# Optimization experiments

Measured on AMD Instinct MI355X. Metric: run time of the kernel, lower is better.

## Reference

```python
import jax, jax.numpy as jnp
import numpy as np
from jax import lax

B = 256; N_LAB = 20000; M = 3; D = 768
T = 5; K = 8; H = 256; DI = 512; S = 16; R = 16; NL = 4; KC = 4


def setup_inputs() -> dict:
    key = jax.random.key(0)
    ks = jax.random.split(key, 16)
    sc = 0.02
    return {
        "unlabeled_embeddings": jax.random.normal(ks[0], (B, M, D), jnp.float32),
        "labeled_embeddings": jax.random.normal(ks[1], (N_LAB, M, D), jnp.float32),
        "labeled_traits": jax.random.uniform(ks[2], (N_LAB, T), jnp.float32),
        "modality_logits": jax.random.normal(ks[3], (T, M), jnp.float32),
        "Wp": jax.random.normal(ks[4], (D + 1, H), jnp.float32) * sc,
        "bp": jnp.zeros((H,), jnp.float32),
        "ln_g": jnp.ones((NL, H), jnp.float32),
        "ln_b": jnp.zeros((NL, H), jnp.float32),
        "Win": jax.random.normal(ks[5], (NL, H, 2 * DI), jnp.float32) * sc,
        "conv_w": jax.random.normal(ks[6], (NL, DI, KC), jnp.float32) * sc,
        "conv_b": jnp.zeros((NL, DI), jnp.float32),
        "Wx": jax.random.normal(ks[7], (NL, DI, R + 2 * S), jnp.float32) * sc,
        "Wdt": jax.random.normal(ks[8], (NL, R, DI), jnp.float32) * sc,
        "bdt": jnp.full((NL, DI), -4.6, jnp.float32),
        "A_log": jnp.log(jnp.broadcast_to(jnp.arange(1, S + 1, dtype=jnp.float32), (NL, DI, S))),
        "Dp": jnp.ones((NL, DI), jnp.float32),
        "Wout": jax.random.normal(ks[9], (NL, DI, H), jnp.float32) * sc,
        "W1": jax.random.normal(ks[10], (H, H // 2), jnp.float32) * sc,
        "b1": jnp.zeros((H // 2,), jnp.float32),
        "W2": jax.random.normal(ks[11], (H // 2, 1), jnp.float32) * sc,
        "b2": jnp.zeros((1,), jnp.float32),
    }


def layer_norm(x, g, b, eps=1e-5):
    m = x.mean(-1, keepdims=True)
    v = ((x - m) ** 2).mean(-1, keepdims=True)
    return (x - m) * lax.rsqrt(v + eps) * g + b


def select_neighbors(lab_e, lab_t, unl_e, mlog):
    # Per-trait modality-weighted cosine similarity k-NN.
    w = jax.nn.softmax(mlog, axis=-1)                       # (T,M)
    q = jnp.einsum('tm,bmd->btd', w, unl_e)                 # (B,T,D)
    kk = jnp.einsum('tm,nmd->ntd', w, lab_e)                # (N,T,D)
    qn = q * lax.rsqrt(jnp.sum(q * q, -1, keepdims=True) + 1e-8)
    kn = kk * lax.rsqrt(jnp.sum(kk * kk, -1, keepdims=True) + 1e-8)
    sim = jnp.einsum('btd,ntd->btn', qn, kn)                # (B,T,N)
    _, idx = lax.top_k(sim, K)                              # (B,T,K) int32
    ne = lab_e[idx]                                         # (B,T,K,M,D)
    tg = lab_t[idx]                                         # (B,T,K,T)
    nt = jnp.diagonal(tg, axis1=1, axis2=3).transpose(0, 2, 1)  # (B,T,K)
    return ne, nt, idx


def mamba_block(x, Win, conv_w, conv_b, Wx, Wdt, bdt, A_log, Dp, Wout):
    # x: (N, L, H). Selective SSM (Mamba) block with internal residual.
    N, L, _ = x.shape
    xz = x @ Win                                            # (N,L,2*DI)
    xc, z = jnp.split(xz, 2, axis=-1)
    xp = jnp.pad(xc, ((0, 0), (KC - 1, 0), (0, 0)))         # causal depthwise conv, k=4
    xc = sum(xp[:, j:j + L, :] * conv_w[:, j] for j in range(KC)) + conv_b
    xc = jax.nn.silu(xc)
    dbl = xc @ Wx                                           # (N,L,R+2S)
    dt, Bm, Cm = jnp.split(dbl, [R, R + S], axis=-1)
    dt = jax.nn.softplus(dt @ Wdt + bdt)                    # (N,L,DI)
    A = -jnp.exp(A_log)                                     # (DI,S)
    dA = jnp.exp(dt[..., None] * A)                         # (N,L,DI,S)
    dBx = dt[..., None] * Bm[:, :, None, :] * xc[..., None] # (N,L,DI,S)

    def step(h, inp):
        a, bx = inp
        h = a * h + bx
        return h, h

    h0 = jnp.zeros((N, DI, S), x.dtype)
    _, hs = lax.scan(step, h0, (jnp.swapaxes(dA, 0, 1), jnp.swapaxes(dBx, 0, 1)))
    hs = jnp.swapaxes(hs, 0, 1)                             # (N,L,DI,S)
    y = jnp.einsum('nlds,nls->nld', hs, Cm) + Dp * xc
    y = y * jax.nn.silu(z)
    return x + y @ Wout


def _forward(unl, lab_e, lab_t, mlog, Wp, bp, ln_g, ln_b, Win, conv_w, conv_b, Wx,
             Wdt, bdt, A_log, Dp, Wout, W1, b1, W2, b2):
    ne, nt, _ = select_neighbors(lab_e, lab_t, unl, mlog)
    ne = ne.mean(3)                                         # (B,T,K,D) mean over modalities
    uc = unl.mean(1)                                        # (B,D)
    feats = jnp.concatenate([ne, jnp.broadcast_to(uc[:, None, None, :], (B, T, 1, D))], axis=2)
    tt = jnp.concatenate([nt[..., None], jnp.zeros((B, T, 1, 1), lab_t.dtype)], axis=2)
    toks = jnp.concatenate([feats, tt], axis=-1).reshape(B * T, K + 1, D + 1)
    x = toks @ Wp + bp                                      # (B*T, K+1, H)
    for i in range(NL):
        xn = layer_norm(x, ln_g[i], ln_b[i])
        x = mamba_block(xn, Win[i], conv_w[i], conv_b[i], Wx[i], Wdt[i], bdt[i],
                        A_log[i], Dp[i], Wout[i])
    ms = x[:, -1, :]                                        # masked-trait token state
    h1 = jax.nn.relu(ms @ W1 + b1)
    return (h1 @ W2 + b2).reshape(B, T)


def reference(unlabeled_embeddings, labeled_embeddings, labeled_traits, modality_logits,
              Wp, bp, ln_g, ln_b, Win, conv_w, conv_b, Wx, Wdt, bdt, A_log, Dp, Wout,
              W1, b1, W2, b2):
    return _forward(unlabeled_embeddings, labeled_embeddings, labeled_traits,
                    modality_logits, Wp, bp, ln_g, ln_b, Win, conv_w, conv_b, Wx,
                    Wdt, bdt, A_log, Dp, Wout, W1, b1, W2, b2)
```

## Files before the change

kernel.cpp:

```cpp
#include <hip/hip_runtime.h>
#include <math.h>

#define B_   256
#define NLAB 20000
#define M_   3
#define D_   768
#define T_   5
#define K_   8
#define H_   256
#define DI_  512
#define S_   16
#define R_   16
#define NL_  4
#define KC_  4
#define L_   9
#define NBT  1280
#define NROW 11520

typedef __attribute__((ext_vector_type(8))) short bf16x8;
typedef __attribute__((ext_vector_type(4))) float floatx4;


__device__ __forceinline__ float block_reduce_sum(float v) {
    __shared__ float red[4];
    int lane = threadIdx.x & 63;
    int wid  = threadIdx.x >> 6;
#pragma unroll
    for (int o = 32; o > 0; o >>= 1) v += __shfl_down(v, o);
    if (lane == 0) red[wid] = v;
    __syncthreads();
    int nw = (int)(blockDim.x >> 6);
    float r = 0.f;
#pragma unroll
    for (int i = 0; i < 4; ++i) if (i < nw) r += red[i];
    __syncthreads();
    return r;
}

__device__ __forceinline__ float sigmoidf_(float x) { return 1.f / (1.f + expf(-x)); }
__device__ __forceinline__ float siluf_(float x)    { return x * sigmoidf_(x); }
__device__ __forceinline__ float softplusf_(float x){ return x > 20.f ? x : log1pf(expf(x)); }

__device__ __forceinline__ unsigned short f2bf(float x) {
    unsigned u = __float_as_uint(x);
    unsigned r = (u + 0x7fffu + ((u >> 16) & 1u)) >> 16;
    return (unsigned short)r;
}
__device__ __forceinline__ float bf2f(unsigned short h) {
    return __uint_as_float(((unsigned)h) << 16);
}


__global__ void k_softmax_w(const float* __restrict__ mlog, float* __restrict__ w) {
    int t = threadIdx.x;
    if (t < T_) {
        float a = mlog[t*M_+0], b = mlog[t*M_+1], c = mlog[t*M_+2];
        float mx = fmaxf(a, fmaxf(b, c));
        float ea = expf(a-mx), eb = expf(b-mx), ec = expf(c-mx);
        float s = ea + eb + ec;
        w[t*M_+0] = ea/s; w[t*M_+1] = eb/s; w[t*M_+2] = ec/s;
    }
}

__global__ __launch_bounds__(256) void k_qn_uc(const float* __restrict__ unl,
                                               const float* __restrict__ w,
                                               unsigned short* __restrict__ qnh,
                                               unsigned short* __restrict__ qnl,
                                               float* __restrict__ uc) {
    int b = blockIdx.x, tid = threadIdx.x;
    float e[3][3];
#pragma unroll
    for (int c = 0; c < 3; ++c) {
        int d = tid + c*256;
#pragma unroll
        for (int m = 0; m < 3; ++m)
            e[c][m] = unl[((size_t)b*3 + m)*D_ + d];
    }
#pragma unroll
    for (int c = 0; c < 3; ++c)
        uc[(size_t)b*D_ + tid + c*256] = (e[c][0] + e[c][1] + e[c][2]) * (1.f/3.f);
    for (int t = 0; t < T_; ++t) {
        float w0 = w[t*3+0], w1 = w[t*3+1], w2 = w[t*3+2];
        float q[3]; float ss = 0.f;
#pragma unroll
        for (int c = 0; c < 3; ++c) {
            q[c] = w0*e[c][0] + w1*e[c][1] + w2*e[c][2];
            ss += q[c]*q[c];
        }
        float tot = block_reduce_sum(ss);
        float inv = rsqrtf(tot + 1e-8f);
#pragma unroll
        for (int c = 0; c < 3; ++c) {
            float v = q[c]*inv;
            size_t o = ((size_t)t*B_ + b)*D_ + tid + c*256;
            unsigned short h = f2bf(v);
            qnh[o] = h; qnl[o] = f2bf(v - bf2f(h));
        }
    }
}

__global__ __launch_bounds__(512) void k_simf(const unsigned short* __restrict__ qnh,
                                              const unsigned short* __restrict__ qnl,
                                              const float* __restrict__ lab_e,
                                              const float* __restrict__ w,
                                              float* __restrict__ sim) {
    __shared__ unsigned short Bh[128*40], Bl[128*40];
    __shared__ float rnl[128];
    int bn = blockIdx.x * 128;
    int t  = blockIdx.y;
    float w0 = w[t*3+0], w1 = w[t*3+1], w2 = w[t*3+2];
    int tid = threadIdx.x;
    int lane = tid & 63, wv = tid >> 6;
    int mbase = (wv >> 1)*64, nbase = (wv & 1)*64;
    int fr = lane & 15, kg = lane >> 4;

    int gr0 = tid >> 3, gr1 = 64 + (tid >> 3), kq = tid & 7;
    int gn0 = bn + gr0, gn1 = bn + gr1;
    bool v0 = gn0 < NLAB, v1 = gn1 < NLAB;
    const float* bp0 = lab_e + (size_t)gn0*(3*D_) + kq*4;
    const float* bp1 = lab_e + (size_t)gn1*(3*D_) + kq*4;

    floatx4 acc[4][4];
#pragma unroll
    for (int mi = 0; mi < 4; ++mi)
#pragma unroll
        for (int ni = 0; ni < 4; ++ni)
            acc[mi][ni] = (floatx4){0.f, 0.f, 0.f, 0.f};

    float ss0 = 0.f, ss1 = 0.f;
    float4 rb0[3], rb1[3];
    float4 z4 = make_float4(0.f, 0.f, 0.f, 0.f);
    rb0[0]=rb0[1]=rb0[2]=z4; rb1[0]=rb1[1]=rb1[2]=z4;
    if (v0) { rb0[0] = *(const float4*)(bp0);
              rb0[1] = *(const float4*)(bp0 + D_);
              rb0[2] = *(const float4*)(bp0 + 2*D_); }
    if (v1) { rb1[0] = *(const float4*)(bp1);
              rb1[1] = *(const float4*)(bp1 + D_);
              rb1[2] = *(const float4*)(bp1 + 2*D_); }

    for (int kt = 0; kt < 24; ++kt) {
        int k0 = kt*32;
        float4 s0, s1;
        s0.x = w0*rb0[0].x + w1*rb0[1].x + w2*rb0[2].x;
        s0.y = w0*rb0[0].y + w1*rb0[1].y + w2*rb0[2].y;
        s0.z = w0*rb0[0].z + w1*rb0[1].z + w2*rb0[2].z;
        s0.w = w0*rb0[0].w + w1*rb0[1].w + w2*rb0[2].w;
        s1.x = w0*rb1[0].x + w1*rb1[1].x + w2*rb1[2].x;
        s1.y = w0*rb1[0].y + w1*rb1[1].y + w2*rb1[2].y;
        s1.z = w0*rb1[0].z + w1*rb1[1].z + w2*rb1[2].z;
        s1.w = w0*rb1[0].w + w1*rb1[1].w + w2*rb1[2].w;
        ss0 += s0.x*s0.x + s0.y*s0.y + s0.z*s0.z + s0.w*s0.w;
        ss1 += s1.x*s1.x + s1.y*s1.y + s1.z*s1.z + s1.w*s1.w;
        ushort4 h0, l0, h1, l1;
        h0.x = f2bf(s0.x); l0.x = f2bf(s0.x - bf2f(h0.x));
        h0.y = f2bf(s0.y); l0.y = f2bf(s0.y - bf2f(h0.y));
        h0.z = f2bf(s0.z); l0.z = f2bf(s0.z - bf2f(h0.z));
        h0.w = f2bf(s0.w); l0.w = f2bf(s0.w - bf2f(h0.w));
        h1.x = f2bf(s1.x); l1.x = f2bf(s1.x - bf2f(h1.x));
        h1.y = f2bf(s1.y); l1.y = f2bf(s1.y - bf2f(h1.y));
        h1.z = f2bf(s1.z); l1.z = f2bf(s1.z - bf2f(h1.z));
        h1.w = f2bf(s1.w); l1.w = f2bf(s1.w - bf2f(h1.w));

        __syncthreads();
        *(ushort4*)(Bh + gr0*40 + kq*4) = h0;
        *(ushort4*)(Bl + gr0*40 + kq*4) = l0;
        *(ushort4*)(Bh + gr1*40 + kq*4) = h1;
        *(ushort4*)(Bl + gr1*40 + kq*4) = l1;
        if (kt < 23) {
            const float* p0 = bp0 + k0 + 32;
            const float* p1 = bp1 + k0 + 32;
            if (v0) { rb0[0] = *(const float4*)(p0);
                      rb0[1] = *(const float4*)(p0 + D_);
                      rb0[2] = *(const float4*)(p0 + 2*D_); }
            if (v1) { rb1[0] = *(const float4*)(p1);
                      rb1[1] = *(const float4*)(p1 + D_);
                      rb1[2] = *(const float4*)(p1 + 2*D_); }
        }
        __syncthreads();

        bf16x8 bhf[4], blf[4];
#pragma unroll
        for (int ni = 0; ni < 4; ++ni) {
            int off = (nbase + ni*16 + fr)*40 + kg*8;
            bhf[ni] = *(const bf16x8*)(Bh + off);
            blf[ni] = *(const bf16x8*)(Bl + off);
        }
#pragma unroll
        for (int mi = 0; mi < 4; ++mi) {
            size_t ga = ((size_t)t*B_ + (mbase + mi*16 + fr))*D_ + k0 + kg*8;
            bf16x8 ahf = *(const bf16x8*)(qnh + ga);
            bf16x8 alf = *(const bf16x8*)(qnl + ga);
#pragma unroll
            for (int ni = 0; ni < 4; ++ni) {
                floatx4 c = acc[mi][ni];
                c = __builtin_amdgcn_mfma_f32_16x16x32_bf16(ahf, bhf[ni], c, 0, 0, 0);
                c = __builtin_amdgcn_mfma_f32_16x16x32_bf16(alf, bhf[ni], c, 0, 0, 0);
                c = __builtin_amdgcn_mfma_f32_16x16x32_bf16(ahf, blf[ni], c, 0, 0, 0);
                acc[mi][ni] = c;
            }
        }
    }

    float t0 = ss0, t1 = ss1;
#pragma unroll
    for (int m = 1; m <= 4; m <<= 1) { t0 += __shfl_xor(t0, m); t1 += __shfl_xor(t1, m); }
    if ((tid & 7) == 0) {
        rnl[tid >> 3]        = rsqrtf(t0 + 1e-8f);
        rnl[64 + (tid >> 3)] = rsqrtf(t1 + 1e-8f);
    }
    __syncthreads();

    float* st = sim + (size_t)t*B_*NLAB;
#pragma unroll
    for (int mi = 0; mi < 4; ++mi) {
        int m = mbase + mi*16 + kg*4;
#pragma unroll
        for (int ni = 0; ni < 4; ++ni) {
            int nl = nbase + ni*16 + fr;
            int n = bn + nl;
            if (n < NLAB) {
                float rv = rnl[nl];
#pragma unroll
                for (int r = 0; r < 4; ++r)
                    st[(size_t)(m + r)*NLAB + n] = acc[mi][ni][r] * rv;
            }
        }
    }
}

__global__ __launch_bounds__(256) void k_topk(const float* __restrict__ sim,
                                              int* __restrict__ idx_out) {
    int b = blockIdx.x;
    int t = blockIdx.y;
    int tid = threadIdx.x;
    const float* row = sim + ((size_t)t*B_ + b)*NLAB;
    float tv[8]; int ti[8];
#pragma unroll
    for (int k = 0; k < 8; ++k) { tv[k] = -3e38f; ti[k] = 0x7fffffff; }
    for (int n = tid; n < NLAB; n += 256) {
        float v = row[n];
        if (v > tv[7]) {
            tv[7] = v; ti[7] = n;
#pragma unroll
            for (int k = 7; k > 0; --k) {
                if (tv[k] > tv[k-1]) {
                    float fv = tv[k]; tv[k] = tv[k-1]; tv[k-1] = fv;
                    int fi = ti[k]; ti[k] = ti[k-1]; ti[k-1] = fi;
                }
            }
        }
    }
    __shared__ float sv[2048];
    __shared__ int   si[2048];
    __shared__ float pv[256];
    __shared__ int   pi[256];
    __shared__ int   pp[256];
#pragma unroll
    for (int k = 0; k < 8; ++k) { sv[tid*8+k] = tv[k]; si[tid*8+k] = ti[k]; }
    __syncthreads();
    for (int r = 0; r < 8; ++r) {
        float bv = -3e38f; int bi = 0x7fffffff; int bp = 0;
#pragma unroll
        for (int k = 0; k < 8; ++k) {
            int p = tid*8 + k;
            float v = sv[p]; int ii = si[p];
            if (v > bv || (v == bv && ii < bi)) { bv = v; bi = ii; bp = p; }
        }
        pv[tid] = bv; pi[tid] = bi; pp[tid] = bp;
        __syncthreads();
        for (int off = 128; off > 0; off >>= 1) {
            if (tid < off) {
                if (pv[tid+off] > pv[tid] || (pv[tid+off] == pv[tid] && pi[tid+off] < pi[tid])) {
                    pv[tid] = pv[tid+off]; pi[tid] = pi[tid+off]; pp[tid] = pp[tid+off];
                }
            }
            __syncthreads();
        }
        if (tid == 0) {
            idx_out[((size_t)b*T_ + t)*K_ + r] = pi[0];
            sv[pp[0]] = -3e38f;
        }
        __syncthreads();
    }
}

__global__ __launch_bounds__(256) void k_toks(const float* __restrict__ lab_e,
                                              const float* __restrict__ lab_t,
                                              const float* __restrict__ uc,
                                              const int* __restrict__ idx,
                                              unsigned short* __restrict__ tokh,
                                              unsigned short* __restrict__ tokl,
                                              float* __restrict__ tt) {
    int g = blockIdx.x;
    int bt = g / L_, l = g % L_;
    int b = bt / T_, t = bt % T_;
    size_t ro = (size_t)g*D_;
    if (l < K_) {
        int n = idx[(size_t)bt*K_ + l];
        for (int d = threadIdx.x; d < D_; d += 256) {
            size_t base = (size_t)n*(3*D_) + d;
            float v = (lab_e[base] + lab_e[base + D_] + lab_e[base + 2*D_]) * (1.f/3.f);
            unsigned short h = f2bf(v);
            tokh[ro + d] = h; tokl[ro + d] = f2bf(v - bf2f(h));
        }
        if (threadIdx.x == 0) tt[g] = lab_t[(size_t)n*T_ + t];
    } else {
        for (int d = threadIdx.x; d < D_; d += 256) {
            float v = uc[(size_t)b*D_ + d];
            unsigned short h = f2bf(v);
            tokh[ro + d] = h; tokl[ro + d] = f2bf(v - bf2f(h));
        }
        if (threadIdx.x == 0) tt[g] = 0.f;
    }
}

__global__ void k_cvtw(const float* __restrict__ W,
                       unsigned short* __restrict__ th,
                       unsigned short* __restrict__ tl,
                       int Kd, int N) {
    int total = Kd * N;
    for (int id = blockIdx.x*256 + threadIdx.x; id < total; id += gridDim.x*256) {
        int n = id / Kd, k = id - n*Kd;
        float v = W[(size_t)k*N + n];
        unsigned short h = f2bf(v);
        th[id] = h; tl[id] = f2bf(v - bf2f(h));
    }
}

template<bool ADD, bool BIAS, bool TRAIT>
__global__ __launch_bounds__(256) void k_mgemm(const unsigned short* __restrict__ ah,
                                               const unsigned short* __restrict__ al,
                                               const unsigned short* __restrict__ bh,
                                               const unsigned short* __restrict__ bl,
                                               const float* __restrict__ bias,
                                               const float* __restrict__ wtrait,
                                               const float* __restrict__ tt,
                                               float* __restrict__ C,
                                               int N, int Kd) {
    __shared__ unsigned short Ah[128*40], Al[128*40], Bh[64*40], Bl[64*40];
    int bn = blockIdx.x * 64;
    int bm = blockIdx.y * 128;
    int tid = threadIdx.x;
    int lane = tid & 63, wv = tid >> 6;
    int mbase = (wv >> 1)*64, nbase = (wv & 1)*32;
    int fr = lane & 15, kg = lane >> 4;
    floatx4 acc[4][2];
#pragma unroll
    for (int mi = 0; mi < 4; ++mi)
#pragma unroll
        for (int ni = 0; ni < 2; ++ni)
            acc[mi][ni] = (floatx4){0.f, 0.f, 0.f, 0.f};

    for (int k0 = 0; k0 < Kd; k0 += 32) {
#pragma unroll
        for (int f = 0; f < 2; ++f) {
            int v = f*256 + tid;
            int r = v >> 2, kq = v & 3;
            size_t g = (size_t)(bm + r)*Kd + k0 + kq*8;
            int off = r*40 + kq*8;
            *(int4*)(Ah + off) = *(const int4*)(ah + g);
            *(int4*)(Al + off) = *(const int4*)(al + g);
        }
        {
            int r = tid >> 2, kq = tid & 3;
            size_t g = (size_t)(bn + r)*Kd + k0 + kq*8;
            int off = r*40 + kq*8;
            *(int4*)(Bh + off) = *(const int4*)(bh + g);
            *(int4*)(Bl + off) = *(const int4*)(bl + g);
        }
        __syncthreads();

        bf16x8 bhf[2], blf[2];
#pragma unroll
        for (int ni = 0; ni < 2; ++ni) {
            int off = (nbase + ni*16 + fr)*40 + kg*8;
            bhf[ni] = *(const bf16x8*)(Bh + off);
            blf[ni] = *(const bf16x8*)(Bl + off);
        }
#pragma unroll
        for (int mi = 0; mi < 4; ++mi) {
            int off = (mbase + mi*16 + fr)*40 + kg*8;
            bf16x8 ahf = *(const bf16x8*)(Ah + off);
            bf16x8 alf = *(const bf16x8*)(Al + off);
#pragma unroll
            for (int ni = 0; ni < 2; ++ni) {
                floatx4 c = acc[mi][ni];
                c = __builtin_amdgcn_mfma_f32_16x16x32_bf16(ahf, bhf[ni], c, 0, 0, 0);
                c = __builtin_amdgcn_mfma_f32_16x16x32_bf16(alf, bhf[ni], c, 0, 0, 0);
                c = __builtin_amdgcn_mfma_f32_16x16x32_bf16(ahf, blf[ni], c, 0, 0, 0);
                acc[mi][ni] = c;
            }
        }
        __syncthreads();
    }
#pragma unroll
    for (int mi = 0; mi < 4; ++mi) {
        int m0 = bm + mbase + mi*16 + kg*4;
#pragma unroll
        for (int ni = 0; ni < 2; ++ni) {
            int n = bn + nbase + ni*16 + fr;
#pragma unroll
            for (int r = 0; r < 4; ++r) {
                float v = acc[mi][ni][r];
                if (TRAIT) v += tt[m0 + r] * wtrait[n];
                if (BIAS)  v += bias[n];
                size_t o = (size_t)(m0 + r)*N + n;
                if (ADD) C[o] += v; else C[o] = v;
            }
        }
    }
}

__global__ __launch_bounds__(256) void k_ln(const float* __restrict__ x,
                                            const float* __restrict__ g,
                                            const float* __restrict__ b,
                                            float* __restrict__ xn,
                                            unsigned short* __restrict__ xnh,
                                            unsigned short* __restrict__ xnl) {
    int row = blockIdx.x, tid = threadIdx.x;
    float v = x[(size_t)row*H_ + tid];
    float mean = block_reduce_sum(v) * (1.f/H_);
    float d = v - mean;
    float var = block_reduce_sum(d*d) * (1.f/H_);
    float o = d * rsqrtf(var + 1e-5f) * g[tid] + b[tid];
    size_t oo = (size_t)row*H_ + tid;
    xn[oo] = o;
    unsigned short h = f2bf(o);
    xnh[oo] = h; xnl[oo] = f2bf(o - bf2f(h));
}

__global__ __launch_bounds__(512) void k_mamba(const float* __restrict__ xz,
                                               const float* __restrict__ cw,
                                               const float* __restrict__ cb,
                                               const unsigned short* __restrict__ wxh,
                                               const unsigned short* __restrict__ wxl,
                                               const float* __restrict__ Wdt,
                                               const float* __restrict__ bdt,
                                               const float* __restrict__ A_log,
                                               const float* __restrict__ Dp,
                                               unsigned short* __restrict__ yh,
                                               unsigned short* __restrict__ yl) {
    __shared__ float xcS[L_][516];
    __shared__ float dblS[L_][48];
    int n = blockIdx.x, d = threadIdx.x;

    float c0 = cw[d*4+0], c1 = cw[d*4+1], c2 = cw[d*4+2], c3 = cw[d*4+3];
    float bb = cb[d];
    const float* src = xz + (size_t)n*L_*(2*DI_) + d;
    float xc[L_], z[L_];
    float x0 = 0.f, x1 = 0.f, x2 = 0.f;
#pragma unroll
    for (int l = 0; l < L_; ++l) {
        float x3 = src[l*(2*DI_)];
        z[l]     = src[l*(2*DI_) + DI_];
        float s = bb + c0*x0 + c1*x1 + c2*x2 + c3*x3;
        float v = siluf_(s);
        xc[l] = v; xcS[l][d] = v;
        x0 = x1; x1 = x2; x2 = x3;
    }
    __syncthreads();

    int wv = d >> 6, lane = d & 63;
    if (wv < 3) {
        int fr = lane & 15, kg = lane >> 4;
        const unsigned short* bph = wxh + (size_t)(wv*16 + fr)*DI_;
        const unsigned short* bpl = wxl + (size_t)(wv*16 + fr)*DI_;
        floatx4 c = (floatx4){0.f, 0.f, 0.f, 0.f};
        for (int k0 = 0; k0 < DI_; k0 += 32) {
            int kb = k0 + kg*8;
            float av[8];
            if (fr < L_) {
                float4 q0 = *(const float4*)(&xcS[fr][kb]);
                float4 q1 = *(const float4*)(&xcS[fr][kb+4]);
                av[0]=q0.x; av[1]=q0.y; av[2]=q0.z; av[3]=q0.w;
                av[4]=q1.x; av[5]=q1.y; av[6]=q1.z; av[7]=q1.w;
            } else {
#pragma unroll
                for (int j = 0; j < 8; ++j) av[j] = 0.f;
            }
            bf16x8 ah, al;
#pragma unroll
            for (int j = 0; j < 8; ++j) {
                unsigned short hh = f2bf(av[j]);
                ah[j] = (short)hh;
                al[j] = (short)f2bf(av[j] - bf2f(hh));
            }
            bf16x8 bhf = *(const bf16x8*)(bph + kb);
            bf16x8 blf = *(const bf16x8*)(bpl + kb);
            c = __builtin_amdgcn_mfma_f32_16x16x32_bf16(ah, bhf, c, 0, 0, 0);
            c = __builtin_amdgcn_mfma_f32_16x16x32_bf16(al, bhf, c, 0, 0, 0);
            c = __builtin_amdgcn_mfma_f32_16x16x32_bf16(ah, blf, c, 0, 0, 0);
        }
#pragma unroll
        for (int r = 0; r < 4; ++r) {
            int row = kg*4 + r;
            if (row < L_) dblS[row][wv*16 + fr] = c[r];
        }
    }
    __syncthreads();

    float a[S_], wdt[R_];
#pragma unroll
    for (int s = 0; s < S_; ++s) a[s] = -expf(A_log[(size_t)d*S_ + s]);
#pragma unroll
    for (int r = 0; r < R_; ++r) wdt[r] = Wdt[(size_t)r*DI_ + d];
    float bdtv = bdt[d], dp = Dp[d];
    float h[S_];
#pragma unroll
    for (int s = 0; s < S_; ++s) h[s] = 0.f;
    size_t ob = (size_t)n*L_*DI_ + d;
#pragma unroll
    for (int l = 0; l < L_; ++l) {
        float s = bdtv;
#pragma unroll
        for (int r = 0; r < R_; ++r) s = fmaf(dblS[l][r], wdt[r], s);
        float dtv = softplusf_(s);
        float xcv = xc[l];
        float accv = 0.f;
#pragma unroll
        for (int si = 0; si < S_; ++si) {
            float Bv = dblS[l][16 + si], Cv = dblS[l][32 + si];
            h[si] = expf(dtv*a[si])*h[si] + dtv*Bv*xcv;
            accv = fmaf(h[si], Cv, accv);
        }
        float yv = (accv + dp*xcv) * siluf_(z[l]);
        unsigned short hh = f2bf(yv);
        yh[ob + (size_t)l*DI_] = hh;
        yl[ob + (size_t)l*DI_] = f2bf(yv - bf2f(hh));
    }
}

__global__ __launch_bounds__(128) void k_head(const float* __restrict__ x,
                                              const float* __restrict__ W1,
                                              const float* __restrict__ b1,
                                              const float* __restrict__ W2,
                                              const float* __restrict__ b2,
                                              float* __restrict__ out) {
    int n = blockIdx.x, tid = threadIdx.x;
    __shared__ float ms[H_];
    const float* src = x + ((size_t)n*L_ + (L_-1))*H_;
    ms[tid] = src[tid];
    ms[tid+128] = src[tid+128];
    __syncthreads();
    float s = b1[tid];
#pragma unroll 8
    for (int k = 0; k < H_; ++k) s = fmaf(ms[k], W1[(size_t)k*128 + tid], s);
    float h = fmaxf(s, 0.f);
    float p = h * W2[tid];
    float tot = block_reduce_sum(p);
    if (tid == 0) out[n] = tot + b2[0];
}


extern "C" void kernel_launch(void* const* d_in, const int* in_sizes, int n_in,
                              void* d_out, int out_size, void* d_ws, size_t ws_size,
                              hipStream_t stream) {
    const float* unl   = (const float*)d_in[0];
    const float* lab_e = (const float*)d_in[1];
    const float* lab_t = (const float*)d_in[2];
    const float* mlog  = (const float*)d_in[3];
    const float* Wp    = (const float*)d_in[4];
    const float* bp    = (const float*)d_in[5];
    const float* ln_g  = (const float*)d_in[6];
    const float* ln_b  = (const float*)d_in[7];
    const float* Win   = (const float*)d_in[8];
    const float* conv_w= (const float*)d_in[9];
    const float* conv_b= (const float*)d_in[10];
    const float* Wx    = (const float*)d_in[11];
    const float* Wdt   = (const float*)d_in[12];
    const float* bdt   = (const float*)d_in[13];
    const float* A_log = (const float*)d_in[14];
    const float* Dp    = (const float*)d_in[15];
    const float* Wout  = (const float*)d_in[16];
    const float* W1    = (const float*)d_in[17];
    const float* b1    = (const float*)d_in[18];
    const float* W2    = (const float*)d_in[19];
    const float* b2    = (const float*)d_in[20];

    float* ws = (float*)d_ws;
    float* w    = ws + 0;
    int*   idx  = (int*)(ws + 16);
    float* uc   = ws + 10256;
    unsigned short* wxth = (unsigned short*)(ws + 206864);
    unsigned short* wxtl = (unsigned short*)(ws + 256016);
    float* tt   = ws + 306864;
    unsigned short* qnh   = (unsigned short*)(ws + 318384);
    unsigned short* qnl   = (unsigned short*)(ws + 809904);
    unsigned short* wph   = (unsigned short*)(ws + 1301424);
    unsigned short* wpl   = (unsigned short*)(ws + 1399728);
    unsigned short* winh  = (unsigned short*)(ws + 1498032);
    unsigned short* winl  = (unsigned short*)(ws + 2022320);
    unsigned short* wouth = (unsigned short*)(ws + 2546608);
    unsigned short* woutl = (unsigned short*)(ws + 2808752);
    float* xa   = ws + 3070896;
    float* xb   = ws + 6020016;
    unsigned short* xnh   = (unsigned short*)(ws + 8969136);
    unsigned short* xnl   = (unsigned short*)(ws + 10443696);
    float* simreg = ws + 18369456;
    float* sim  = simreg;
    float* xz   = simreg;
    unsigned short* tokh = (unsigned short*)(simreg + 11796480);
    unsigned short* tokl = (unsigned short*)(simreg + 16220160);
    unsigned short* yh   = (unsigned short*)(simreg + 17694720);
    unsigned short* yl   = (unsigned short*)(simreg + 20643840);

    k_softmax_w<<<1, 64, 0, stream>>>(mlog, w);
    k_qn_uc<<<B_, 256, 0, stream>>>(unl, w, qnh, qnl, uc);
    k_cvtw<<<(768*256 + 255)/256, 256, 0, stream>>>(Wp, wph, wpl, 768, 256);
    for (int i = 0; i < NL_; ++i) {
        k_cvtw<<<(256*1024 + 255)/256, 256, 0, stream>>>(Win + (size_t)i*H_*(2*DI_),
                                                         winh + (size_t)i*H_*(2*DI_),
                                                         winl + (size_t)i*H_*(2*DI_), 256, 1024);
        k_cvtw<<<(512*256 + 255)/256, 256, 0, stream>>>(Wout + (size_t)i*DI_*H_,
                                                        wouth + (size_t)i*DI_*H_,
                                                        woutl + (size_t)i*DI_*H_, 512, 256);
        k_cvtw<<<(512*48 + 255)/256, 256, 0, stream>>>(Wx + (size_t)i*DI_*48,
                                                       wxth + (size_t)i*48*DI_,
                                                       wxtl + (size_t)i*48*DI_, 512, 48);
    }
    {
        dim3 g((NLAB + 127) / 128, T_);
        k_simf<<<g, 512, 0, stream>>>(qnh, qnl, lab_e, w, sim);
    }
    {
        dim3 g(B_, T_);
        k_topk<<<g, 256, 0, stream>>>(sim, idx);
    }
    k_toks<<<NROW, 256, 0, stream>>>(lab_e, lab_t, uc, idx, tokh, tokl, tt);
    {
        dim3 g(H_/64, NROW/128);
        k_mgemm<false,true,true><<<g, 256, 0, stream>>>(tokh, tokl, wph, wpl,
                                                        bp, Wp + (size_t)768*H_, tt, xa, H_, D_);
    }
    float* cur = xa;
    float* oth = xb;
    for (int i = 0; i < NL_; ++i) {
        k_ln<<<NROW, 256, 0, stream>>>(cur, ln_g + (size_t)i*H_, ln_b + (size_t)i*H_, oth, xnh, xnl);
        {
            dim3 g((2*DI_)/64, NROW/128);
            k_mgemm<false,false,false><<<g, 256, 0, stream>>>(xnh, xnl,
                winh + (size_t)i*H_*(2*DI_), winl + (size_t)i*H_*(2*DI_),
                nullptr, nullptr, nullptr, xz, 2*DI_, H_);
        }
        k_mamba<<<NBT, 512, 0, stream>>>(xz,
                                         conv_w + (size_t)i*DI_*KC_, conv_b + (size_t)i*DI_,
                                         wxth + (size_t)i*48*DI_, wxtl + (size_t)i*48*DI_,
                                         Wdt + (size_t)i*R_*DI_, bdt + (size_t)i*DI_,
                                         A_log + (size_t)i*DI_*S_, Dp + (size_t)i*DI_,
                                         yh, yl);
        {
            dim3 g(H_/64, NROW/128);
            k_mgemm<true,false,false><<<g, 256, 0, stream>>>(yh, yl,
                wouth + (size_t)i*DI_*H_, woutl + (size_t)i*DI_*H_,
                nullptr, nullptr, nullptr, oth, H_, DI_);
        }
        float* tmp = cur; cur = oth; oth = tmp;
    }
    k_head<<<NBT, 128, 0, stream>>>(cur, W1, b1, W2, b2, (float*)d_out);
}
```

Measured before the change: 1.521 ms.

## Double-buffer LDS in similarity GEMM, prefetch A fragments, remap blocks per XCD

```diff
diff --git a/kernel.cpp b/kernel.cpp
--- a/kernel.cpp
+++ b/kernel.cpp
@@ -50,6 +50,11 @@
     return __uint_as_float(((unsigned)h) << 16);
 }
 
+__device__ __forceinline__ void barrier_lds_only() {
+    asm volatile("s_waitcnt lgkmcnt(0)" ::: "memory");
+    __builtin_amdgcn_s_barrier();
+}
+
 
 __global__ void k_softmax_w(const float* __restrict__ mlog, float* __restrict__ w) {
     int t = threadIdx.x;
@@ -99,15 +104,40 @@
     }
 }
 
-__global__ __launch_bounds__(512) void k_simf(const unsigned short* __restrict__ qnh,
-                                              const unsigned short* __restrict__ qnl,
-                                              const float* __restrict__ lab_e,
-                                              const float* __restrict__ w,
-                                              float* __restrict__ sim) {
-    __shared__ unsigned short Bh[128*40], Bl[128*40];
+__device__ __forceinline__ void cvt_store4(const float4* rb, float w0, float w1, float w2,
+                                           unsigned short* bh, unsigned short* bl,
+                                           int off, float& ss) {
+    float4 s;
+    s.x = w0*rb[0].x + w1*rb[1].x + w2*rb[2].x;
+    s.y = w0*rb[0].y + w1*rb[1].y + w2*rb[2].y;
+    s.z = w0*rb[0].z + w1*rb[1].z + w2*rb[2].z;
+    s.w = w0*rb[0].w + w1*rb[1].w + w2*rb[2].w;
+    ss += s.x*s.x + s.y*s.y + s.z*s.z + s.w*s.w;
+    ushort4 h, l;
+    h.x = f2bf(s.x); l.x = f2bf(s.x - bf2f(h.x));
+    h.y = f2bf(s.y); l.y = f2bf(s.y - bf2f(h.y));
+    h.z = f2bf(s.z); l.z = f2bf(s.z - bf2f(h.z));
+    h.w = f2bf(s.w); l.w = f2bf(s.w - bf2f(h.w));
+    *(ushort4*)(bh + off) = h;
+    *(ushort4*)(bl + off) = l;
+}
+
+__global__ __launch_bounds__(512, 4) void k_simf(const unsigned short* __restrict__ qnh,
+                                                 const unsigned short* __restrict__ qnl,
+                                                 const float* __restrict__ lab_e,
+                                                 const float* __restrict__ w,
+                                                 float* __restrict__ sim) {
+    __shared__ unsigned short Bh[2*128*40], Bl[2*128*40];
     __shared__ float rnl[128];
-    int bn = blockIdx.x * 128;
-    int t  = blockIdx.y;
+    int bid = blockIdx.x;
+    int xcd = bid & 7, s = bid >> 3;
+    int cnt = (xcd < 5) ? 20 : 19;
+    if (s >= cnt * 5) return;
+    int start = (xcd < 5) ? xcd*20 : 100 + (xcd-5)*19;
+    int bnc = start + s / 5;
+    int t = s - (s/5)*5;
+    int bn = bnc * 128;
+
     float w0 = w[t*3+0], w1 = w[t*3+1], w2 = w[t*3+2];
     int tid = threadIdx.x;
     int lane = tid & 63, wv = tid >> 6;
@@ -137,35 +167,26 @@
     if (v1) { rb1[0] = *(const float4*)(bp1);
               rb1[1] = *(const float4*)(bp1 + D_);
               rb1[2] = *(const float4*)(bp1 + 2*D_); }
+    cvt_store4(rb0, w0, w1, w2, Bh, Bl, gr0*40 + kq*4, ss0);
+    cvt_store4(rb1, w0, w1, w2, Bh, Bl, gr1*40 + kq*4, ss1);
+
+    const unsigned short* aph = qnh + ((size_t)t*B_ + mbase + fr)*D_ + kg*8;
+    const unsigned short* apl = qnl + ((size_t)t*B_ + mbase + fr)*D_ + kg*8;
 
     for (int kt = 0; kt < 24; ++kt) {
+        int cur = kt & 1;
+        const unsigned short* bhr = Bh + cur*5120;
+        const unsigned short* blr = Bl + cur*5120;
+        unsigned short* bhw = Bh + (cur^1)*5120;
+        unsigned short* blw = Bl + (cur^1)*5120;
         int k0 = kt*32;
-        float4 s0, s1;
-        s0.x = w0*rb0[0].x + w1*rb0[1].x + w2*rb0[2].x;
-        s0.y = w0*rb0[0].y + w1*rb0[1].y + w2*rb0[2].y;
-        s0.z = w0*rb0[0].z + w1*rb0[1].z + w2*rb0[2].z;
-        s0.w = w0*rb0[0].w + w1*rb0[1].w + w2*rb0[2].w;
-        s1.x = w0*rb1[0].x + w1*rb1[1].x + w2*rb1[2].x;
-        s1.y = w0*rb1[0].y + w1*rb1[1].y + w2*rb1[2].y;
-        s1.z = w0*rb1[0].z + w1*rb1[1].z + w2*rb1[2].z;
-        s1.w = w0*rb1[0].w + w1*rb1[1].w + w2*rb1[2].w;
-        ss0 += s0.x*s0.x + s0.y*s0.y + s0.z*s0.z + s0.w*s0.w;
-        ss1 += s1.x*s1.x + s1.y*s1.y + s1.z*s1.z + s1.w*s1.w;
-        ushort4 h0, l0, h1, l1;
-        h0.x = f2bf(s0.x); l0.x = f2bf(s0.x - bf2f(h0.x));
-        h0.y = f2bf(s0.y); l0.y = f2bf(s0.y - bf2f(h0.y));
-        h0.z = f2bf(s0.z); l0.z = f2bf(s0.z - bf2f(h0.z));
-        h0.w = f2bf(s0.w); l0.w = f2bf(s0.w - bf2f(h0.w));
-        h1.x = f2bf(s1.x); l1.x = f2bf(s1.x - bf2f(h1.x));
-        h1.y = f2bf(s1.y); l1.y = f2bf(s1.y - bf2f(h1.y));
-        h1.z = f2bf(s1.z); l1.z = f2bf(s1.z - bf2f(h1.z));
-        h1.w = f2bf(s1.w); l1.w = f2bf(s1.w - bf2f(h1.w));
-
-        __syncthreads();
-        *(ushort4*)(Bh + gr0*40 + kq*4) = h0;
-        *(ushort4*)(Bl + gr0*40 + kq*4) = l0;
-        *(ushort4*)(Bh + gr1*40 + kq*4) = h1;
-        *(ushort4*)(Bl + gr1*40 + kq*4) = l1;
+
+        bf16x8 ahf[4], alf[4];
+#pragma unroll
+        for (int mi = 0; mi < 4; ++mi) {
+            ahf[mi] = *(const bf16x8*)(aph + (size_t)mi*16*D_ + k0);
+            alf[mi] = *(const bf16x8*)(apl + (size_t)mi*16*D_ + k0);
+        }
         if (kt < 23) {
             const float* p0 = bp0 + k0 + 32;
             const float* p1 = bp1 + k0 + 32;
@@ -176,28 +197,30 @@
                       rb1[1] = *(const float4*)(p1 + D_);
                       rb1[2] = *(const float4*)(p1 + 2*D_); }
         }
-        __syncthreads();
+
+        barrier_lds_only();
 
         bf16x8 bhf[4], blf[4];
 #pragma unroll
         for (int ni = 0; ni < 4; ++ni) {
             int off = (nbase + ni*16 + fr)*40 + kg*8;
-            bhf[ni] = *(const bf16x8*)(Bh + off);
-            blf[ni] = *(const bf16x8*)(Bl + off);
+            bhf[ni] = *(const bf16x8*)(bhr + off);
+            blf[ni] = *(const bf16x8*)(blr + off);
         }
 #pragma unroll
         for (int mi = 0; mi < 4; ++mi) {
-            size_t ga = ((size_t)t*B_ + (mbase + mi*16 + fr))*D_ + k0 + kg*8;
-            bf16x8 ahf = *(const bf16x8*)(qnh + ga);
-            bf16x8 alf = *(const bf16x8*)(qnl + ga);
 #pragma unroll
             for (int ni = 0; ni < 4; ++ni) {
                 floatx4 c = acc[mi][ni];
-                c = __builtin_amdgcn_mfma_f32_16x16x32_bf16(ahf, bhf[ni], c, 0, 0, 0);
-                c = __builtin_amdgcn_mfma_f32_16x16x32_bf16(alf, bhf[ni], c, 0, 0, 0);
-                c = __builtin_amdgcn_mfma_f32_16x16x32_bf16(ahf, blf[ni], c, 0, 0, 0);
+                c = __builtin_amdgcn_mfma_f32_16x16x32_bf16(ahf[mi], bhf[ni], c, 0, 0, 0);
+                c = __builtin_amdgcn_mfma_f32_16x16x32_bf16(alf[mi], bhf[ni], c, 0, 0, 0);
+                c = __builtin_amdgcn_mfma_f32_16x16x32_bf16(ahf[mi], blf[ni], c, 0, 0, 0);
                 acc[mi][ni] = c;
             }
+        }
+        if (kt < 23) {
+            cvt_store4(rb0, w0, w1, w2, bhw, blw, gr0*40 + kq*4, ss0);
+            cvt_store4(rb1, w0, w1, w2, bhw, blw, gr1*40 + kq*4, ss1);
         }
     }
 
@@ -618,10 +641,7 @@
                                                        wxth + (size_t)i*48*DI_,
                                                        wxtl + (size_t)i*48*DI_, 512, 48);
     }
-    {
-        dim3 g((NLAB + 127) / 128, T_);
-        k_simf<<<g, 512, 0, stream>>>(qnh, qnl, lab_e, w, sim);
-    }
+    k_simf<<<800, 512, 0, stream>>>(qnh, qnl, lab_e, w, sim);
     {
         dim3 g(B_, T_);
         k_topk<<<g, 256, 0, stream>>>(sim, idx);
```

Result: slower. 1.912 ms (+25.7%).
